# Kernel tuning notes

Measured on AMD Instinct MI355X. Metric: run time of the kernel, lower is better.

The kernel has to match this reference:

```python
import jax, jax.numpy as jnp
import numpy as np

KY, KX = 3, 3  # kernel_size from init_kwargs


def setup_inputs() -> dict:
    key = jax.random.key(0)
    x = jax.random.normal(key, (8, 32, 512, 512), dtype=jnp.float32)
    return {"x": x}


def reference(x):
    # Replicate-pad H by (KY-1)//2, W by (KX-1)//2 (matches F.pad mode='replicate').
    py, px = (KY - 1) // 2, (KX - 1) // 2
    B, C, H, W = x.shape
    padded = jnp.pad(x, ((0, 0), (0, 0), (py, py), (px, px)), mode='edge')
    center = (KY * KX) // 2
    # The torch module builds an identity neigh2channel kernel with the center
    # tap zeroed, then maxes over the KY*KX channels. The zeroed center channel
    # contributes a constant 0 to that max, so we initialize the running max at 0
    # and fold in every non-center neighbor via shifted slices (no blown-up
    # [B,C,KY*KX,H,W] tensor is materialized).
    m = jnp.zeros_like(x)
    for idx in range(KY * KX):
        if idx == center:
            continue
        i, j = divmod(idx, KX)
        m = jnp.maximum(m, padded[:, :, i:i + H, j:j + W])
    mask = (x > m).astype(x.dtype)
    return x * mask
```

## Files before the change

### kernel.cpp

```cpp
#include <hip/hip_runtime.h>


#define IMG_W 512
#define IMG_H 512
#define TILE_H 4
#define THREADS 256
#define SROWS (TILE_H + 2)
#define SSTRIDE 520

static_assert((SROWS * (IMG_W / 4)) % THREADS == 0, "staging divides evenly");
static_assert(IMG_W % THREADS == 0, "compute strips divide evenly");
static_assert(IMG_H % TILE_H == 0, "tiles divide evenly");

__global__ __launch_bounds__(THREADS)
void nms3x3_kernel(const float* __restrict__ x, float* __restrict__ out) {
    const int tile = blockIdx.x;
    const int bc   = blockIdx.y;
    const int h0   = tile * TILE_H;
    const float* img  = x   + (size_t)bc * IMG_H * IMG_W;
    float*       oimg = out + (size_t)bc * IMG_H * IMG_W;

    __shared__ float sh[SROWS * SSTRIDE];

    const int tid = threadIdx.x;

    constexpr int NVEC = SROWS * (IMG_W / 4);
    constexpr int ITERS = NVEC / THREADS;
#pragma unroll
    for (int k = 0; k < ITERS; ++k) {
        const int i  = tid + k * THREADS;
        const int r  = i >> 7;
        const int c4 = i & 127;
        int gh = h0 - 1 + r;
        gh = max(0, min(IMG_H - 1, gh));
        const float4 v = *(const float4*)(img + (size_t)gh * IMG_W + (c4 << 2));
        *(float4*)(&sh[r * SSTRIDE + (c4 << 2)]) = v;
    }
    __syncthreads();

#pragma unroll
    for (int s = 0; s < IMG_W / THREADS; ++s) {
        const int c  = tid + s * THREADS;
        const int cl = (c == 0)         ? 0         : c - 1;
        const int cr = (c == IMG_W - 1) ? IMG_W - 1 : c + 1;

        float lv[SROWS], mv[SROWS], rv[SROWS];
#pragma unroll
        for (int rr = 0; rr < SROWS; ++rr) {
            lv[rr] = sh[rr * SSTRIDE + cl];
            mv[rr] = sh[rr * SSTRIDE + c];
            rv[rr] = sh[rr * SSTRIDE + cr];
        }
#pragma unroll
        for (int k = 0; k < TILE_H; ++k) {
            float mx = 0.0f;
            mx = fmaxf(mx, lv[k]);     mx = fmaxf(mx, lv[k + 1]); mx = fmaxf(mx, lv[k + 2]);
            mx = fmaxf(mx, mv[k]);                                 mx = fmaxf(mx, mv[k + 2]);
            mx = fmaxf(mx, rv[k]);     mx = fmaxf(mx, rv[k + 1]); mx = fmaxf(mx, rv[k + 2]);
            const float cen = mv[k + 1];
            oimg[(size_t)(h0 + k) * IMG_W + c] = (cen > mx) ? cen : 0.0f;
        }
    }
}

extern "C" void kernel_launch(void* const* d_in, const int* in_sizes, int n_in,
                              void* d_out, int out_size, void* d_ws, size_t ws_size,
                              hipStream_t stream) {
    const float* x  = (const float*)d_in[0];
    float* out      = (float*)d_out;
    dim3 grid(IMG_H / TILE_H, 8 * 32);
    nms3x3_kernel<<<grid, dim3(THREADS), 0, stream>>>(x, out);
}
```

Measured before the change: 423.4 us.

## Replace shared-memory staging with register sliding window over rows

Drops the LDS tile and __syncthreads. Each thread now owns four columns over eight consecutive rows and keeps the row-wise horizontal maxima in registers as it slides down, loading neighbouring edge scalars straight from global memory. Output stores become float4-vectorized, and the separable max reuses the horizontal max across rows. The cost is halo rows reread by each 8-row strip and extra scalar global loads for the left and right neighbours, which should mostly hit cache.

```diff
diff --git a/kernel.cpp b/kernel.cpp
--- a/kernel.cpp
+++ b/kernel.cpp
@@ -3,71 +3,64 @@
 
 #define IMG_W 512
 #define IMG_H 512
-#define TILE_H 4
+#define RPT 8
 #define THREADS 256
-#define SROWS (TILE_H + 2)
-#define SSTRIDE 520
 
-static_assert((SROWS * (IMG_W / 4)) % THREADS == 0, "staging divides evenly");
-static_assert(IMG_W % THREADS == 0, "compute strips divide evenly");
-static_assert(IMG_H % TILE_H == 0, "tiles divide evenly");
+__device__ __forceinline__ float4 vmax4(float4 a, float4 b) {
+    return make_float4(fmaxf(a.x, b.x), fmaxf(a.y, b.y),
+                       fmaxf(a.z, b.z), fmaxf(a.w, b.w));
+}
 
 __global__ __launch_bounds__(THREADS)
 void nms3x3_kernel(const float* __restrict__ x, float* __restrict__ out) {
-    const int tile = blockIdx.x;
-    const int bc   = blockIdx.y;
-    const int h0   = tile * TILE_H;
-    const float* img  = x   + (size_t)bc * IMG_H * IMG_W;
-    float*       oimg = out + (size_t)bc * IMG_H * IMG_W;
+    const int cg   = threadIdx.x & 127;
+    const int half = threadIdx.x >> 7;
+    const int c0   = cg << 2;
+    const int r0   = blockIdx.x * (2 * RPT) + half * RPT;
+    const size_t plane = (size_t)blockIdx.y * IMG_H * IMG_W;
+    const float* img  = x + plane;
+    float*       oimg = out + plane;
 
-    __shared__ float sh[SROWS * SSTRIDE];
+    const int cl = (c0 == 0) ? 0 : c0 - 1;
+    const int cr = (c0 + 4 >= IMG_W) ? IMG_W - 1 : c0 + 4;
 
-    const int tid = threadIdx.x;
+    auto loadrow = [&](int r, float4& h3o, float4& h2o, float4& vo) {
+        r = min(IMG_H - 1, max(0, r));
+        const float* rowp = img + (size_t)r * IMG_W;
+        const float4 v  = *(const float4*)(rowp + c0);
+        const float  sL = rowp[cl];
+        const float  sR = rowp[cr];
+        const float4 l  = make_float4(sL, v.x, v.y, v.z);
+        const float4 rr = make_float4(v.y, v.z, v.w, sR);
+        h2o = vmax4(l, rr);
+        h3o = vmax4(h2o, v);
+        vo  = v;
+    };
 
-    constexpr int NVEC = SROWS * (IMG_W / 4);
-    constexpr int ITERS = NVEC / THREADS;
-#pragma unroll
-    for (int k = 0; k < ITERS; ++k) {
-        const int i  = tid + k * THREADS;
-        const int r  = i >> 7;
-        const int c4 = i & 127;
-        int gh = h0 - 1 + r;
-        gh = max(0, min(IMG_H - 1, gh));
-        const float4 v = *(const float4*)(img + (size_t)gh * IMG_W + (c4 << 2));
-        *(float4*)(&sh[r * SSTRIDE + (c4 << 2)]) = v;
-    }
-    __syncthreads();
+    float4 h3p, h2p, vp, h3c, h2c, vc, h3n, h2n, vn;
+    loadrow(r0 - 1, h3p, h2p, vp);
+    loadrow(r0,     h3c, h2c, vc);
 
 #pragma unroll
-    for (int s = 0; s < IMG_W / THREADS; ++s) {
-        const int c  = tid + s * THREADS;
-        const int cl = (c == 0)         ? 0         : c - 1;
-        const int cr = (c == IMG_W - 1) ? IMG_W - 1 : c + 1;
-
-        float lv[SROWS], mv[SROWS], rv[SROWS];
-#pragma unroll
-        for (int rr = 0; rr < SROWS; ++rr) {
-            lv[rr] = sh[rr * SSTRIDE + cl];
-            mv[rr] = sh[rr * SSTRIDE + c];
-            rv[rr] = sh[rr * SSTRIDE + cr];
-        }
-#pragma unroll
-        for (int k = 0; k < TILE_H; ++k) {
-            float mx = 0.0f;
-            mx = fmaxf(mx, lv[k]);     mx = fmaxf(mx, lv[k + 1]); mx = fmaxf(mx, lv[k + 2]);
-            mx = fmaxf(mx, mv[k]);                                 mx = fmaxf(mx, mv[k + 2]);
-            mx = fmaxf(mx, rv[k]);     mx = fmaxf(mx, rv[k + 1]); mx = fmaxf(mx, rv[k + 2]);
-            const float cen = mv[k + 1];
-            oimg[(size_t)(h0 + k) * IMG_W + c] = (cen > mx) ? cen : 0.0f;
-        }
+    for (int k = 0; k < RPT; ++k) {
+        loadrow(r0 + k + 1, h3n, h2n, vn);
+        float4 m8 = vmax4(vmax4(h3p, h3n), h2c);
+        float4 o;
+        o.x = (vc.x > fmaxf(m8.x, 0.0f)) ? vc.x : 0.0f;
+        o.y = (vc.y > fmaxf(m8.y, 0.0f)) ? vc.y : 0.0f;
+        o.z = (vc.z > fmaxf(m8.z, 0.0f)) ? vc.z : 0.0f;
+        o.w = (vc.w > fmaxf(m8.w, 0.0f)) ? vc.w : 0.0f;
+        *(float4*)(oimg + (size_t)(r0 + k) * IMG_W + c0) = o;
+        h3p = h3c; h2p = h2c; vp = vc;
+        h3c = h3n; h2c = h2n; vc = vn;
     }
 }
 
 extern "C" void kernel_launch(void* const* d_in, const int* in_sizes, int n_in,
                               void* d_out, int out_size, void* d_ws, size_t ws_size,
                               hipStream_t stream) {
-    const float* x  = (const float*)d_in[0];
-    float* out      = (float*)d_out;
-    dim3 grid(IMG_H / TILE_H, 8 * 32);
+    const float* x = (const float*)d_in[0];
+    float* out     = (float*)d_out;
+    dim3 grid(IMG_H / (2 * RPT), 8 * 32);
     nms3x3_kernel<<<grid, dim3(THREADS), 0, stream>>>(x, out);
 }
```

After: 426.9 us. About the same (+0.8%).
